# Performance work log

Measured on AMD Instinct MI355X. Metric: run time of the kernel, lower is better.

## Reference

```python
import jax, jax.numpy as jnp
import numpy as np

B, T_ENC, H_ENC, H_DEC, ATTN = 64, 4096, 512, 512, 256


def setup_inputs() -> dict:
    key = jax.random.key(0)
    k1, k2, k3, k4, k5 = jax.random.split(key, 5)
    decoder_state = jax.random.normal(k1, (B, H_DEC), dtype=jnp.float32)
    encoder_outputs = jax.random.normal(k2, (B, T_ENC, H_ENC), dtype=jnp.float32)
    # nn.Linear(in, out, bias=False) weight has shape (out, in); apply as x @ W.T
    W_enc = jax.random.normal(k3, (ATTN, H_ENC), dtype=jnp.float32) * (1.0 / np.sqrt(H_ENC))
    W_dec = jax.random.normal(k4, (ATTN, H_DEC), dtype=jnp.float32) * (1.0 / np.sqrt(H_DEC))
    v = jax.random.normal(k5, (1, ATTN), dtype=jnp.float32) * (1.0 / np.sqrt(ATTN))
    return {"decoder_state": decoder_state, "encoder_outputs": encoder_outputs,
            "W_enc": W_enc, "W_dec": W_dec, "v": v}


def reference(decoder_state, encoder_outputs, W_enc, W_dec, v):
    # enc_proj: (B, T, A); dec_proj: (B, 1, A)
    enc_proj = jnp.einsum('bte,ae->bta', encoder_outputs, W_enc)
    dec_proj = jnp.einsum('bd,ad->ba', decoder_state, W_dec)[:, None, :]
    energy = jnp.tanh(enc_proj + dec_proj)              # (B, T, A)
    scores = jnp.einsum('bta,a->bt', energy, v[0])      # (B, T)
    attn_weights = jax.nn.softmax(scores, axis=1)       # (B, T)
    context = jnp.einsum('bte,bt->be', encoder_outputs, attn_weights)  # (B, H_enc)
    return context, attn_weights
```

## Files before the change

### kernel.cpp

```cpp
#include <hip/hip_runtime.h>
#include <hip/hip_bf16.h>

#define B 64
#define T_ENC 4096
#define H_ENC 512
#define H_DEC 512
#define ATTN 256

#define BM 64
#define BK 32
#define LDA 40

typedef __attribute__((ext_vector_type(8))) short bf16x8;
typedef __attribute__((ext_vector_type(4))) float f32x4;

__device__ __forceinline__ unsigned short f2bf(float f) {
    unsigned int u = __float_as_uint(f);
    unsigned int rounding = 0x7fffu + ((u >> 16) & 1u);
    return (unsigned short)((u + rounding) >> 16);
}

__device__ __forceinline__ float fast_tanh(float x) {
    float ax = fabsf(x);
    float e = __expf(2.0f * fminf(ax, 15.0f));
    float t = 1.0f - 2.0f / (e + 1.0f);
    return copysignf(t, x);
}

__global__ void convw_kernel(const float* __restrict__ W,
                             unsigned short* __restrict__ out) {
    int i = (blockIdx.x * 256 + threadIdx.x) * 4;
    float4 x = *(const float4*)(W + i);
    ushort4 u;
    u.x = f2bf(x.x); u.y = f2bf(x.y); u.z = f2bf(x.z); u.w = f2bf(x.w);
    *(ushort4*)(out + i) = u;
}

__global__ void decproj_kernel(const float* __restrict__ dec,
                               const float* __restrict__ Wdec,
                               float* __restrict__ dproj) {
    __shared__ float sdec[H_DEC];
    int b = blockIdx.x;
    int tid = threadIdx.x;
    sdec[tid]       = dec[b * H_DEC + tid];
    sdec[tid + 256] = dec[b * H_DEC + tid + 256];
    __syncthreads();
    const float* wrow = Wdec + (size_t)tid * H_DEC;
    float acc = 0.0f;
#pragma unroll 4
    for (int k = 0; k < H_DEC; k += 4) {
        float4 w4 = *(const float4*)(wrow + k);
        acc += w4.x * sdec[k] + w4.y * sdec[k + 1] + w4.z * sdec[k + 2] + w4.w * sdec[k + 3];
    }
    dproj[b * ATTN + tid] = acc;
}

__global__ __launch_bounds__(256) void fused_kernel(
    const float* __restrict__ enc,
    const unsigned short* __restrict__ wencb,
    const float* __restrict__ dproj,
    const float* __restrict__ v,
    float* __restrict__ scores,
    float* __restrict__ ctxp,
    float* __restrict__ ml)
{
    __shared__ unsigned short Abuf[BM * LDA];
    __shared__ unsigned short Bbuf[ATTN * LDA];
    __shared__ float sPart[BM * 4];
    __shared__ float sP[BM];

    const int tid  = threadIdx.x;
    const int wave = tid >> 6;
    const int lane = tid & 63;
    const int quad = lane >> 4;
    const int l16  = lane & 15;
    const int chunk = blockIdx.x;
    const int m0   = chunk * BM;
    const int b    = m0 >> 12;

    f32x4 acc[4][4];
#pragma unroll
    for (int mi = 0; mi < 4; ++mi)
#pragma unroll
        for (int ni = 0; ni < 4; ++ni) {
            f32x4 z = {0.0f, 0.0f, 0.0f, 0.0f};
            acc[mi][ni] = z;
        }

    for (int k0 = 0; k0 < H_ENC; k0 += BK) {
#pragma unroll
        for (int rep = 0; rep < 2; ++rep) {
            int idx = rep * 1024 + tid * 4;
            int r = idx >> 5, c = idx & 31;
            float4 x = *(const float4*)(enc + (size_t)(m0 + r) * H_ENC + k0 + c);
            ushort4 u;
            u.x = f2bf(x.x); u.y = f2bf(x.y); u.z = f2bf(x.z); u.w = f2bf(x.w);
            *(ushort4*)(&Abuf[r * LDA + c]) = u;
        }
#pragma unroll
        for (int rep = 0; rep < 4; ++rep) {
            int chnk = rep * 256 + tid;
            int r = chnk >> 2, off = (chnk & 3) * 8;
            bf16x8 x = *(const bf16x8*)(wencb + (size_t)r * H_ENC + k0 + off);
            *(bf16x8*)(&Bbuf[r * LDA + off]) = x;
        }
        __syncthreads();

        bf16x8 afrag[4], bfrag[4];
#pragma unroll
        for (int mi = 0; mi < 4; ++mi)
            afrag[mi] = *(const bf16x8*)(&Abuf[(mi * 16 + l16) * LDA + quad * 8]);
#pragma unroll
        for (int ni = 0; ni < 4; ++ni)
            bfrag[ni] = *(const bf16x8*)(&Bbuf[(wave * 64 + ni * 16 + l16) * LDA + quad * 8]);

#pragma unroll
        for (int mi = 0; mi < 4; ++mi)
#pragma unroll
            for (int ni = 0; ni < 4; ++ni)
                acc[mi][ni] = __builtin_amdgcn_mfma_f32_16x16x32_bf16(
                    afrag[mi], bfrag[ni], acc[mi][ni], 0, 0, 0);
        __syncthreads();
    }

    float decp[4], vv[4];
#pragma unroll
    for (int ni = 0; ni < 4; ++ni) {
        int a = wave * 64 + ni * 16 + l16;
        decp[ni] = dproj[b * ATTN + a];
        vv[ni]   = v[a];
    }
#pragma unroll
    for (int mi = 0; mi < 4; ++mi) {
#pragma unroll
        for (int r = 0; r < 4; ++r) {
            float sum = 0.0f;
#pragma unroll
            for (int ni = 0; ni < 4; ++ni) {
                float x = acc[mi][ni][r] + decp[ni];
                sum += fast_tanh(x) * vv[ni];
            }
            sum += __shfl_xor(sum, 1);
            sum += __shfl_xor(sum, 2);
            sum += __shfl_xor(sum, 4);
            sum += __shfl_xor(sum, 8);
            if (l16 == 0) {
                int m = mi * 16 + quad * 4 + r;
                sPart[m * 4 + wave] = sum;
            }
        }
    }
    __syncthreads();

    if (tid < BM) {
        float s = sPart[tid * 4 + 0] + sPart[tid * 4 + 1] +
                  sPart[tid * 4 + 2] + sPart[tid * 4 + 3];
        scores[m0 + tid] = s;
        float m = s;
#pragma unroll
        for (int o = 1; o < 64; o <<= 1) m = fmaxf(m, __shfl_xor(m, o));
        float p = __expf(s - m);
        float l = p;
#pragma unroll
        for (int o = 1; o < 64; o <<= 1) l += __shfl_xor(l, o);
        sP[tid] = p;
        if (tid == 0) {
            ml[chunk * 2]     = m;
            ml[chunk * 2 + 1] = l;
        }
    }
    __syncthreads();

    int e0 = tid * 2;
    const float* ebase = enc + (size_t)m0 * H_ENC + e0;
    float cx = 0.0f, cy = 0.0f;
#pragma unroll 4
    for (int t = 0; t < BM; ++t) {
        float wt = sP[t];
        float2 x = *(const float2*)(ebase + (size_t)t * H_ENC);
        cx += wt * x.x;
        cy += wt * x.y;
    }
    float* cp = ctxp + (size_t)chunk * H_ENC + e0;
    cp[0] = cx;
    cp[1] = cy;
}

__global__ __launch_bounds__(256) void combine_kernel(
    const float* __restrict__ scores,
    const float* __restrict__ ctxp,
    const float* __restrict__ ml,
    float* __restrict__ out)
{
    __shared__ float sc[64];
    __shared__ float sML[2];
    const int b = blockIdx.x;
    const int tid = threadIdx.x;
    const int nch = T_ENC / BM;

    if (tid < nch) {
        float m = ml[(b * nch + tid) * 2];
        float l = ml[(b * nch + tid) * 2 + 1];
        float M = m;
#pragma unroll
        for (int o = 1; o < 64; o <<= 1) M = fmaxf(M, __shfl_xor(M, o));
        float scale = __expf(m - M);
        float contrib = l * scale;
        float L = contrib;
#pragma unroll
        for (int o = 1; o < 64; o <<= 1) L += __shfl_xor(L, o);
        sc[tid] = scale;
        if (tid == 0) { sML[0] = M; sML[1] = L; }
    }
    __syncthreads();
    const float M = sML[0];
    const float invL = 1.0f / sML[1];

    const float* sb = scores + (size_t)b * T_ENC;
    float* attn = out + B * H_ENC + (size_t)b * T_ENC;
#pragma unroll
    for (int i = 0; i < 16; ++i) {
        int t = i * 256 + tid;
        attn[t] = __expf(sb[t] - M) * invL;
    }

    int e0 = tid * 2;
    const float* cp = ctxp + ((size_t)b * nch) * H_ENC + e0;
    float cx = 0.0f, cy = 0.0f;
#pragma unroll 4
    for (int i = 0; i < nch; ++i) {
        float s = sc[i];
        float2 x = *(const float2*)(cp + (size_t)i * H_ENC);
        cx += s * x.x;
        cy += s * x.y;
    }
    out[b * H_ENC + e0]     = cx * invL;
    out[b * H_ENC + e0 + 1] = cy * invL;
}

extern "C" void kernel_launch(void* const* d_in, const int* in_sizes, int n_in,
                              void* d_out, int out_size, void* d_ws, size_t ws_size,
                              hipStream_t stream) {
    const float* dec  = (const float*)d_in[0];
    const float* enc  = (const float*)d_in[1];
    const float* Wenc = (const float*)d_in[2];
    const float* Wdec = (const float*)d_in[3];
    const float* v    = (const float*)d_in[4];
    float* out = (float*)d_out;
    float* ws  = (float*)d_ws;

    const int NCHUNK = (B * T_ENC) / BM;

    float* scores = ws;
    float* dproj  = scores + (size_t)B * T_ENC;
    unsigned short* wencb = (unsigned short*)(dproj + B * ATTN);
    float* ctxp = dproj + B * ATTN + (ATTN * H_ENC) / 2;
    float* ml   = ctxp + (size_t)NCHUNK * H_ENC;

    hipLaunchKernelGGL(convw_kernel, dim3((ATTN * H_ENC) / 1024), dim3(256), 0, stream,
                       Wenc, wencb);
    hipLaunchKernelGGL(decproj_kernel, dim3(B), dim3(256), 0, stream, dec, Wdec, dproj);
    hipLaunchKernelGGL(fused_kernel, dim3(NCHUNK), dim3(256), 0, stream,
                       enc, wencb, dproj, v, scores, ctxp, ml);
    hipLaunchKernelGGL(combine_kernel, dim3(B), dim3(256), 0, stream,
                       scores, ctxp, ml, out);
}
```

Before: 871.1 us.

## Enlarge GEMM tile to 128x256 with swizzled direct-to-LDS weight loads

Doubles the rows per block to 128 and K-step to 64, using a 2x2 wave layout so each wave computes a 64x128 sub-tile. The weight is pre-tiled and XOR-swizzled in the conversion kernel so it can be loaded straight into LDS with global_load_lds, and it uses packed bf16 conversion intrinsics. The aim is to halve the number of times the W_enc tile is reloaded per row and to cut LDS bank conflicts and conversion overhead. The in-block softmax is reworked to span two waves and the combine kernel is adjusted for 32 chunks per batch. In exchange, the larger accumulator raises register pressure, which may limit occupancy.

Result: faster. 788.0 us (-9.5%).

```diff
diff --git a/kernel.cpp b/kernel.cpp
--- a/kernel.cpp
+++ b/kernel.cpp
@@ -7,17 +7,18 @@
 #define H_DEC 512
 #define ATTN 256
 
-#define BM 64
-#define BK 32
-#define LDA 40
+#define BM 128
+#define BK 64
+#define LDA_A 72
+#define NCH_PER_B (T_ENC / BM)
+#define NCHUNKS ((B * T_ENC) / BM)
 
 typedef __attribute__((ext_vector_type(8))) short bf16x8;
 typedef __attribute__((ext_vector_type(4))) float f32x4;
 
-__device__ __forceinline__ unsigned short f2bf(float f) {
-    unsigned int u = __float_as_uint(f);
-    unsigned int rounding = 0x7fffu + ((u >> 16) & 1u);
-    return (unsigned short)((u + rounding) >> 16);
+__device__ __forceinline__ ushort2 cvt2_bf16(float x, float y) {
+    __hip_bfloat162 h = __float22bfloat162_rn(make_float2(x, y));
+    return *reinterpret_cast<ushort2*>(&h);
 }
 
 __device__ __forceinline__ float fast_tanh(float x) {
@@ -27,13 +28,30 @@
     return copysignf(t, x);
 }
 
+__device__ __forceinline__ void gload_lds16(const void* g, void* l) {
+    __builtin_amdgcn_global_load_lds(
+        (const __attribute__((address_space(1))) void*)g,
+        (__attribute__((address_space(3))) void*)l, 16, 0, 0);
+}
+
 __global__ void convw_kernel(const float* __restrict__ W,
                              unsigned short* __restrict__ out) {
-    int i = (blockIdx.x * 256 + threadIdx.x) * 4;
-    float4 x = *(const float4*)(W + i);
-    ushort4 u;
-    u.x = f2bf(x.x); u.y = f2bf(x.y); u.z = f2bf(x.z); u.w = f2bf(x.w);
-    *(ushort4*)(out + i) = u;
+    int g = blockIdx.x * 256 + threadIdx.x;
+    int j = g & 7;
+    int r = (g >> 3) & 255;
+    int t = g >> 11;
+    int c0 = t * 64 + ((j ^ (r & 7)) << 3);
+    const float* src = W + (size_t)r * H_ENC + c0;
+    float4 x0 = *(const float4*)(src);
+    float4 x1 = *(const float4*)(src + 4);
+    ushort2 a0 = cvt2_bf16(x0.x, x0.y);
+    ushort2 a1 = cvt2_bf16(x0.z, x0.w);
+    ushort2 a2 = cvt2_bf16(x1.x, x1.y);
+    ushort2 a3 = cvt2_bf16(x1.z, x1.w);
+    ushort4 lo = {a0.x, a0.y, a1.x, a1.y};
+    ushort4 hi = {a2.x, a2.y, a3.x, a3.y};
+    *(ushort4*)(out + (size_t)g * 8)     = lo;
+    *(ushort4*)(out + (size_t)g * 8 + 4) = hi;
 }
 
 __global__ void decproj_kernel(const float* __restrict__ dec,
@@ -55,7 +73,7 @@
     dproj[b * ATTN + tid] = acc;
 }
 
-__global__ __launch_bounds__(256) void fused_kernel(
+__global__ __launch_bounds__(256, 2) void fused_kernel(
     const float* __restrict__ enc,
     const unsigned short* __restrict__ wencb,
     const float* __restrict__ dproj,
@@ -64,69 +82,88 @@
     float* __restrict__ ctxp,
     float* __restrict__ ml)
 {
-    __shared__ unsigned short Abuf[BM * LDA];
-    __shared__ unsigned short Bbuf[ATTN * LDA];
-    __shared__ float sPart[BM * 4];
+    __shared__ __align__(16) unsigned short Abuf[BM * LDA_A];
+    __shared__ __align__(16) unsigned short Bbuf[ATTN * BK];
+    __shared__ float sPart[BM * 2];
     __shared__ float sP[BM];
+    __shared__ float sW[4];
 
     const int tid  = threadIdx.x;
     const int wave = tid >> 6;
     const int lane = tid & 63;
     const int quad = lane >> 4;
     const int l16  = lane & 15;
+    const int wr   = wave >> 1;
+    const int wc   = wave & 1;
+    const int swz  = (l16 & 7) << 4;
     const int chunk = blockIdx.x;
     const int m0   = chunk * BM;
-    const int b    = m0 >> 12;
-
-    f32x4 acc[4][4];
+    const int b    = chunk >> 5;
+
+    f32x4 acc[4][8];
 #pragma unroll
     for (int mi = 0; mi < 4; ++mi)
 #pragma unroll
-        for (int ni = 0; ni < 4; ++ni) {
+        for (int ni = 0; ni < 8; ++ni) {
             f32x4 z = {0.0f, 0.0f, 0.0f, 0.0f};
             acc[mi][ni] = z;
         }
 
+    const char* wb = (const char*)wencb;
+    char* bb = (char*)Bbuf;
+
     for (int k0 = 0; k0 < H_ENC; k0 += BK) {
-#pragma unroll
-        for (int rep = 0; rep < 2; ++rep) {
-            int idx = rep * 1024 + tid * 4;
-            int r = idx >> 5, c = idx & 31;
-            float4 x = *(const float4*)(enc + (size_t)(m0 + r) * H_ENC + k0 + c);
-            ushort4 u;
-            u.x = f2bf(x.x); u.y = f2bf(x.y); u.z = f2bf(x.z); u.w = f2bf(x.w);
-            *(ushort4*)(&Abuf[r * LDA + c]) = u;
-        }
-#pragma unroll
-        for (int rep = 0; rep < 4; ++rep) {
-            int chnk = rep * 256 + tid;
-            int r = chnk >> 2, off = (chnk & 3) * 8;
-            bf16x8 x = *(const bf16x8*)(wencb + (size_t)r * H_ENC + k0 + off);
-            *(bf16x8*)(&Bbuf[r * LDA + off]) = x;
+        const int t = k0 >> 6;
+#pragma unroll
+        for (int i = 0; i < 8; ++i) {
+            int u = i * 256 + tid;
+            gload_lds16(wb + (((size_t)t * 2048 + u) << 4), bb + (u << 4));
+        }
+#pragma unroll
+        for (int rp = 0; rp < 4; ++rp) {
+            int idx = rp * 2048 + tid * 8;
+            int r = idx >> 6, c = idx & 63;
+            const float* p = enc + (size_t)(m0 + r) * H_ENC + k0 + c;
+            float4 x0 = *(const float4*)(p);
+            float4 x1 = *(const float4*)(p + 4);
+            ushort2 a0 = cvt2_bf16(x0.x, x0.y);
+            ushort2 a1 = cvt2_bf16(x0.z, x0.w);
+            ushort2 a2 = cvt2_bf16(x1.x, x1.y);
+            ushort2 a3 = cvt2_bf16(x1.z, x1.w);
+            union { bf16x8 v8; unsigned short u[8]; } U;
+            U.u[0] = a0.x; U.u[1] = a0.y; U.u[2] = a1.x; U.u[3] = a1.y;
+            U.u[4] = a2.x; U.u[5] = a2.y; U.u[6] = a3.x; U.u[7] = a3.y;
+            *(bf16x8*)(&Abuf[r * LDA_A + c]) = U.v8;
         }
         __syncthreads();
 
-        bf16x8 afrag[4], bfrag[4];
-#pragma unroll
-        for (int mi = 0; mi < 4; ++mi)
-            afrag[mi] = *(const bf16x8*)(&Abuf[(mi * 16 + l16) * LDA + quad * 8]);
-#pragma unroll
-        for (int ni = 0; ni < 4; ++ni)
-            bfrag[ni] = *(const bf16x8*)(&Bbuf[(wave * 64 + ni * 16 + l16) * LDA + quad * 8]);
-
-#pragma unroll
-        for (int mi = 0; mi < 4; ++mi)
-#pragma unroll
-            for (int ni = 0; ni < 4; ++ni)
-                acc[mi][ni] = __builtin_amdgcn_mfma_f32_16x16x32_bf16(
-                    afrag[mi], bfrag[ni], acc[mi][ni], 0, 0, 0);
+#pragma unroll
+        for (int kk = 0; kk < 2; ++kk) {
+            bf16x8 af[4], bfv[8];
+            const int ca = kk * 32 + quad * 8;
+            const int dc = kk * 64 + quad * 16;
+#pragma unroll
+            for (int mi = 0; mi < 4; ++mi)
+                af[mi] = *(const bf16x8*)(&Abuf[(wr * 64 + mi * 16 + l16) * LDA_A + ca]);
+#pragma unroll
+            for (int ni = 0; ni < 8; ++ni) {
+                int a = wc * 128 + ni * 16 + l16;
+                bfv[ni] = *(const bf16x8*)(bb + a * 128 + (dc ^ swz));
+            }
+#pragma unroll
+            for (int mi = 0; mi < 4; ++mi)
+#pragma unroll
+                for (int ni = 0; ni < 8; ++ni)
+                    acc[mi][ni] = __builtin_amdgcn_mfma_f32_16x16x32_bf16(
+                        af[mi], bfv[ni], acc[mi][ni], 0, 0, 0);
+        }
         __syncthreads();
     }
 
-    float decp[4], vv[4];
-#pragma unroll
-    for (int ni = 0; ni < 4; ++ni) {
-        int a = wave * 64 + ni * 16 + l16;
+    float decp[8], vv[8];
+#pragma unroll
+    for (int ni = 0; ni < 8; ++ni) {
+        int a = wc * 128 + ni * 16 + l16;
         decp[ni] = dproj[b * ATTN + a];
         vv[ni]   = v[a];
     }
@@ -136,48 +173,49 @@
         for (int r = 0; r < 4; ++r) {
             float sum = 0.0f;
 #pragma unroll
-            for (int ni = 0; ni < 4; ++ni) {
-                float x = acc[mi][ni][r] + decp[ni];
-                sum += fast_tanh(x) * vv[ni];
-            }
+            for (int ni = 0; ni < 8; ++ni)
+                sum += fast_tanh(acc[mi][ni][r] + decp[ni]) * vv[ni];
             sum += __shfl_xor(sum, 1);
             sum += __shfl_xor(sum, 2);
             sum += __shfl_xor(sum, 4);
             sum += __shfl_xor(sum, 8);
-            if (l16 == 0) {
-                int m = mi * 16 + quad * 4 + r;
-                sPart[m * 4 + wave] = sum;
-            }
-        }
-    }
-    __syncthreads();
-
-    if (tid < BM) {
-        float s = sPart[tid * 4 + 0] + sPart[tid * 4 + 1] +
-                  sPart[tid * 4 + 2] + sPart[tid * 4 + 3];
+            if (l16 == 0)
+                sPart[(wr * 64 + mi * 16 + quad * 4 + r) * 2 + wc] = sum;
+        }
+    }
+    __syncthreads();
+
+    const bool act = tid < BM;
+    float s = -INFINITY;
+    if (act) {
+        s = sPart[tid * 2] + sPart[tid * 2 + 1];
         scores[m0 + tid] = s;
-        float m = s;
-#pragma unroll
-        for (int o = 1; o < 64; o <<= 1) m = fmaxf(m, __shfl_xor(m, o));
-        float p = __expf(s - m);
-        float l = p;
-#pragma unroll
-        for (int o = 1; o < 64; o <<= 1) l += __shfl_xor(l, o);
-        sP[tid] = p;
-        if (tid == 0) {
-            ml[chunk * 2]     = m;
-            ml[chunk * 2 + 1] = l;
-        }
-    }
-    __syncthreads();
+    }
+    float m = s;
+#pragma unroll
+    for (int o = 1; o < 64; o <<= 1) m = fmaxf(m, __shfl_xor(m, o));
+    if (act && lane == 0) sW[wave] = m;
+    __syncthreads();
+    const float M = fmaxf(sW[0], sW[1]);
+    float p = act ? __expf(s - M) : 0.0f;
+    float l = p;
+#pragma unroll
+    for (int o = 1; o < 64; o <<= 1) l += __shfl_xor(l, o);
+    if (act && lane == 0) sW[2 + wave] = l;
+    if (act) sP[tid] = p;
+    __syncthreads();
+    if (tid == 0) {
+        ml[chunk * 2]     = M;
+        ml[chunk * 2 + 1] = sW[2] + sW[3];
+    }
 
     int e0 = tid * 2;
     const float* ebase = enc + (size_t)m0 * H_ENC + e0;
     float cx = 0.0f, cy = 0.0f;
-#pragma unroll 4
-    for (int t = 0; t < BM; ++t) {
-        float wt = sP[t];
-        float2 x = *(const float2*)(ebase + (size_t)t * H_ENC);
+#pragma unroll 8
+    for (int tt = 0; tt < BM; ++tt) {
+        float wt = sP[tt];
+        float2 x = *(const float2*)(ebase + (size_t)tt * H_ENC);
         cx += wt * x.x;
         cy += wt * x.y;
     }
@@ -192,24 +230,26 @@
     const float* __restrict__ ml,
     float* __restrict__ out)
 {
-    __shared__ float sc[64];
+    __shared__ float sc[NCH_PER_B];
     __shared__ float sML[2];
     const int b = blockIdx.x;
     const int tid = threadIdx.x;
-    const int nch = T_ENC / BM;
-
+    const int nch = NCH_PER_B;
+
+    float m_in = -INFINITY, l_in = 0.0f;
     if (tid < nch) {
-        float m = ml[(b * nch + tid) * 2];
-        float l = ml[(b * nch + tid) * 2 + 1];
-        float M = m;
-#pragma unroll
-        for (int o = 1; o < 64; o <<= 1) M = fmaxf(M, __shfl_xor(M, o));
-        float scale = __expf(m - M);
-        float contrib = l * scale;
-        float L = contrib;
-#pragma unroll
-        for (int o = 1; o < 64; o <<= 1) L += __shfl_xor(L, o);
-        sc[tid] = scale;
+        m_in = ml[(b * nch + tid) * 2];
+        l_in = ml[(b * nch + tid) * 2 + 1];
+    }
+    if (tid < 64) {
+        float M = m_in;
+#pragma unroll
+        for (int o = 1; o < 32; o <<= 1) M = fmaxf(M, __shfl_xor(M, o));
+        float scale = (tid < nch) ? __expf(m_in - M) : 0.0f;
+        float L = l_in * scale;
+#pragma unroll
+        for (int o = 1; o < 32; o <<= 1) L += __shfl_xor(L, o);
+        if (tid < nch) sc[tid] = scale;
         if (tid == 0) { sML[0] = M; sML[1] = L; }
     }
     __syncthreads();
@@ -229,10 +269,10 @@
     float cx = 0.0f, cy = 0.0f;
 #pragma unroll 4
     for (int i = 0; i < nch; ++i) {
-        float s = sc[i];
+        float s2 = sc[i];
         float2 x = *(const float2*)(cp + (size_t)i * H_ENC);
-        cx += s * x.x;
-        cy += s * x.y;
+        cx += s2 * x.x;
+        cy += s2 * x.y;
     }
     out[b * H_ENC + e0]     = cx * invL;
     out[b * H_ENC + e0 + 1] = cy * invL;
@@ -249,18 +289,16 @@
     float* out = (float*)d_out;
     float* ws  = (float*)d_ws;
 
-    const int NCHUNK = (B * T_ENC) / BM;
-
     float* scores = ws;
     float* dproj  = scores + (size_t)B * T_ENC;
     unsigned short* wencb = (unsigned short*)(dproj + B * ATTN);
     float* ctxp = dproj + B * ATTN + (ATTN * H_ENC) / 2;
-    float* ml   = ctxp + (size_t)NCHUNK * H_ENC;
-
-    hipLaunchKernelGGL(convw_kernel, dim3((ATTN * H_ENC) / 1024), dim3(256), 0, stream,
+    float* ml   = ctxp + (size_t)NCHUNKS * H_ENC;
+
+    hipLaunchKernelGGL(convw_kernel, dim3((ATTN * H_ENC) / (256 * 8)), dim3(256), 0, stream,
                        Wenc, wencb);
     hipLaunchKernelGGL(decproj_kernel, dim3(B), dim3(256), 0, stream, dec, Wdec, dproj);
-    hipLaunchKernelGGL(fused_kernel, dim3(NCHUNK), dim3(256), 0, stream,
+    hipLaunchKernelGGL(fused_kernel, dim3(NCHUNKS), dim3(256), 0, stream,
                        enc, wencb, dproj, v, scores, ctxp, ml);
     hipLaunchKernelGGL(combine_kernel, dim3(B), dim3(256), 0, stream,
                        scores, ctxp, ml, out);
```
